# Performance work log

Measured on AMD Instinct MI355X. Metric: run time of the kernel, lower is better.

Reference implementation:

```python
import jax, jax.numpy as jnp
import numpy as np

BATCH = 32768
TEXT_DIM = 384
HIDDEN = 256
NUM_LAYERS = 4
NUM_VERTS = 12
K_NN = 6


def _build_template():
    """Icosphere vertices (12, normalized) and row-normalized kNN adjacency (12,12)."""
    phi = (1.0 + 5.0 ** 0.5) / 2.0
    v = np.array([
        [-1, phi, 0], [1, phi, 0], [-1, -phi, 0], [1, -phi, 0],
        [0, -1, phi], [0, 1, phi], [0, -1, -phi], [0, 1, -phi],
        [phi, 0, -1], [phi, 0, 1], [-phi, 0, -1], [-phi, 0, 1],
    ], dtype=np.float32)
    v = v / np.linalg.norm(v, axis=1, keepdims=True)
    dist = np.linalg.norm(v[:, None, :] - v[None, :, :], axis=-1)  # (12,12)
    # k+1 smallest per row; index 0 is self (distance 0), skip it
    idx = np.argsort(dist, axis=1, kind='stable')[:, 1:K_NN + 1]
    adj = np.zeros((NUM_VERTS, NUM_VERTS), dtype=np.float32)
    rows = np.repeat(np.arange(NUM_VERTS), K_NN)
    adj[rows, idx.reshape(-1)] = 1.0
    adj = adj / (adj.sum(axis=1, keepdims=True) + 1e-6)
    return jnp.asarray(v), jnp.asarray(adj)


def setup_inputs() -> dict:
    key = jax.random.key(0)
    ks = jax.random.split(key, 8)
    template, adjacency = _build_template()
    scale = 0.02
    return {
        "text_emb": jax.random.normal(ks[0], (BATCH, TEXT_DIM), dtype=jnp.float32),
        "W_text": jax.random.normal(ks[1], (TEXT_DIM, HIDDEN), dtype=jnp.float32) * scale,
        "b_text": jnp.zeros((HIDDEN,), dtype=jnp.float32),
        "W_gnn": jax.random.normal(ks[2], (NUM_LAYERS, HIDDEN, HIDDEN), dtype=jnp.float32) * scale,
        "b_gnn": jnp.zeros((NUM_LAYERS, HIDDEN), dtype=jnp.float32),
        "W_out": jax.random.normal(ks[3], (HIDDEN, 3), dtype=jnp.float32) * scale,
        "b_out": jnp.zeros((3,), dtype=jnp.float32),
        "adjacency": adjacency,   # (12,12) buffer
        "template": template,     # (12,3) buffer
    }


def reference(text_emb, W_text, b_text, W_gnn, b_gnn, W_out, b_out, adjacency, template):
    # text projection -> broadcast to all nodes
    tf = text_emb @ W_text + b_text                       # (B, H)
    B = text_emb.shape[0]
    h = jnp.broadcast_to(tf[:, None, :], (B, NUM_VERTS, HIDDEN))
    # GNN layers: aggregate (shared adjacency across batch), project, relu
    for l in range(NUM_LAYERS):
        agg = jnp.einsum('nm,bmd->bnd', adjacency, h)     # (B, 12, H)
        h = jax.nn.relu(agg @ W_gnn[l] + b_gnn[l])
    displacements = h @ W_out + b_out                     # (B, 12, 3)
    return template[None, :, :] + displacements
```

## Files before the change

### kernel.cpp

```cpp
#include <hip/hip_runtime.h>
#include <stdint.h>

#define TD      384
#define HID     256
#define NLAYERS 4

typedef __bf16 bf16;
typedef __attribute__((ext_vector_type(8))) __bf16 bf16x8;
typedef __attribute__((ext_vector_type(4))) float f32x4;

union FragU { uint4 u; bf16x8 f; };
union PackU { uint4 u; bf16 v[8]; };

__device__ inline f32x4 mfma16(bf16x8 a, bf16x8 b, f32x4 c) {
  return __builtin_amdgcn_mfma_f32_16x16x32_bf16(a, b, c, 0, 0, 0);
}

__global__ __launch_bounds__(256) void prep_kernel(
    const float* __restrict__ W_text, const float* __restrict__ W_gnn,
    const float* __restrict__ W_out,
    bf16* __restrict__ wt_text, bf16* __restrict__ wt_gnn, float* __restrict__ wot)
{
  int bid = blockIdx.x, tid = threadIdx.x;
  if (bid < 48) {
    int idx = bid * 256 + tid;
    int cc = idx & 15, c = idx >> 4;
    int n16 = c / 48, oct = c - n16 * 48;
    int n = n16 * 16 + cc;
    PackU pk;
    #pragma unroll
    for (int j = 0; j < 8; j++) pk.v[j] = (bf16)W_text[(oct * 8 + j) * HID + n];
    *(uint4*)(wt_text + idx * 8) = pk.u;
  } else if (bid < 176) {
    int idx = (bid - 48) * 256 + tid;
    int cc = idx & 15, c = idx >> 4;
    int l = c >> 9, c2 = c & 511;
    int oct = c2 & 31;
    int n = (c2 >> 5) * 16 + cc;
    const float* base = W_gnn + l * HID * HID;
    PackU pk;
    #pragma unroll
    for (int j = 0; j < 8; j++) pk.v[j] = (bf16)base[(oct * 8 + j) * HID + n];
    *(uint4*)(wt_gnn + idx * 8) = pk.u;
  } else {
    for (int t = tid; t < 3 * HID; t += 256) {
      int comp = t >> 8, k = t & 255;
      wot[comp * HID + k] = W_out[k * 3 + comp];
    }
  }
}

__global__ __launch_bounds__(256, 2) void mesh_kernel(
    const float* __restrict__ text,
    const bf16* __restrict__ wt_text,
    const bf16* __restrict__ wt_gnn,
    const float* __restrict__ b_text,
    const float* __restrict__ b_gnn,
    const float* __restrict__ wot,
    const float* __restrict__ b_out,
    const float* __restrict__ tmpl,
    float* __restrict__ out)
{
  __shared__ __align__(16) unsigned char smem[81920];
  unsigned char* Tbuf = smem;
  unsigned char* Hbuf = smem + 49152;

  const int tid  = threadIdx.x;
  const int lane = tid & 63;
  const int w    = tid >> 6;
  const int cc   = lane & 15;
  const int qq   = lane >> 4;
  const int rowbase = blockIdx.x * 64;

  f32x4 acc[4][4];

  {
    const float* tbase = text + (size_t)rowbase * TD;
    #pragma unroll
    for (int i = 0; i < 12; i++) {
      int id = i * 256 + tid;
      int m = id / 48, o = id - m * 48;
      const float4* p = (const float4*)(tbase + m * TD + o * 8);
      float4 x = p[0], y = p[1];
      PackU pk;
      pk.v[0]=(bf16)x.x; pk.v[1]=(bf16)x.y; pk.v[2]=(bf16)x.z; pk.v[3]=(bf16)x.w;
      pk.v[4]=(bf16)y.x; pk.v[5]=(bf16)y.y; pk.v[6]=(bf16)y.z; pk.v[7]=(bf16)y.w;
      *(uint4*)(Tbuf + m * 768 + (o ^ (m & 7)) * 16) = pk.u;
    }
  }
  __syncthreads();

  auto zero_acc = [&]() {
    f32x4 z = {0.f, 0.f, 0.f, 0.f};
    #pragma unroll
    for (int mt = 0; mt < 4; mt++)
      #pragma unroll
      for (int nt = 0; nt < 4; nt++) acc[mt][nt] = z;
  };

  auto loadA = [&](const unsigned char* src, int rowB, int ks, bf16x8* A) {
    #pragma unroll
    for (int mt = 0; mt < 4; mt++) {
      int m = mt * 16 + cc;
      FragU fu;
      fu.u = *(const uint4*)(src + m * rowB + (((ks * 4 + qq) ^ (m & 7)) * 16));
      A[mt] = fu.f;
    }
  };

  auto loadB = [&](const char* wb, int K8, int ks, bf16x8* B) {
    #pragma unroll
    for (int nt = 0; nt < 4; nt++) {
      FragU fu;
      fu.u = *(const uint4*)(wb + (size_t)(nt * K8 + ks * 4) * 256);
      B[nt] = fu.f;
    }
  };

  auto runLayer = [&](const unsigned char* src, int rowB, int nks,
                      const char* wb, int K8,
                      unsigned char* dst, const float* bias_ptr, bool relu) {
    zero_acc();
    bf16x8 A[4], B[4], An[4], Bn[4];
    loadB(wb, K8, 0, B);
    loadA(src, rowB, 0, A);
    #pragma unroll
    for (int ks = 0; ks < nks; ks++) {
      if (ks + 1 < nks) {
        loadB(wb, K8, ks + 1, Bn);
        loadA(src, rowB, ks + 1, An);
      }
      #pragma unroll
      for (int mt = 0; mt < 4; mt++)
        #pragma unroll
        for (int nt = 0; nt < 4; nt++)
          acc[mt][nt] = mfma16(A[mt], B[nt], acc[mt][nt]);
      if (ks + 1 < nks) {
        #pragma unroll
        for (int t = 0; t < 4; t++) { A[t] = An[t]; B[t] = Bn[t]; }
      }
    }
    float bias4[4];
    #pragma unroll
    for (int nt = 0; nt < 4; nt++) bias4[nt] = bias_ptr[w * 64 + nt * 16 + cc];
    #pragma unroll
    for (int mt = 0; mt < 4; mt++) {
      #pragma unroll
      for (int nt = 0; nt < 4; nt++) {
        int col = w * 64 + nt * 16 + cc;
        #pragma unroll
        for (int r = 0; r < 4; r++) {
          int m = mt * 16 + qq * 4 + r;
          float v = acc[mt][nt][r] + bias4[nt];
          if (relu) v = fmaxf(v, 0.f);
          *(bf16*)(dst + m * 512 + ((col >> 3) ^ (m & 7)) * 16 + (col & 7) * 2) = (bf16)v;
        }
      }
    }
  };

  const char* wb0 = (const char*)wt_text + (size_t)(w * 4 * 48 + qq) * 256 + cc * 16;

  runLayer(Tbuf, 768, TD / 32, wb0, 48, Hbuf, b_text, false);
  __syncthreads();

  #pragma unroll
  for (int l = 0; l < NLAYERS; l++) {
    const unsigned char* src = (l & 1) ? Tbuf : Hbuf;
    unsigned char*       dst = (l & 1) ? Hbuf : Tbuf;
    const char* wb = (const char*)(wt_gnn) + (size_t)l * HID * HID * 2
                   + (size_t)(w * 4 * 32 + qq) * 256 + cc * 16;
    runLayer(src, 512, HID / 32, wb, 32, dst, b_gnn + l * HID, true);
    __syncthreads();
  }

  float* dispBuf = (float*)Tbuf;

  if (tid < 192) {
    int comp = tid >> 6;
    int r = tid & 63;
    const float4* wrow = (const float4*)(wot + comp * HID);
    float s = 0.f;
    #pragma unroll 4
    for (int o = 0; o < 32; o++) {
      FragU fu; fu.u = *(const uint4*)(Hbuf + r * 512 + ((o ^ (r & 7)) * 16));
      float4 w0 = wrow[2 * o], w1 = wrow[2 * o + 1];
      s += (float)fu.f[0]*w0.x + (float)fu.f[1]*w0.y + (float)fu.f[2]*w0.z + (float)fu.f[3]*w0.w;
      s += (float)fu.f[4]*w1.x + (float)fu.f[5]*w1.y + (float)fu.f[6]*w1.z + (float)fu.f[7]*w1.w;
    }
    dispBuf[r * 3 + comp] = s + b_out[comp];
  }
  __syncthreads();

  #pragma unroll
  for (int ii = 0; ii < 9; ii++) {
    int i = ii * 256 + tid;
    int row = i / 36;
    int j = i - row * 36;
    out[(size_t)rowbase * 36 + i] = tmpl[j] + dispBuf[row * 3 + j % 3];
  }
}

extern "C" void kernel_launch(void* const* d_in, const int* in_sizes, int n_in,
                              void* d_out, int out_size, void* d_ws, size_t ws_size,
                              hipStream_t stream) {
  const float* text   = (const float*)d_in[0];
  const float* W_text = (const float*)d_in[1];
  const float* b_text = (const float*)d_in[2];
  const float* W_gnn  = (const float*)d_in[3];
  const float* b_gnn  = (const float*)d_in[4];
  const float* W_out  = (const float*)d_in[5];
  const float* b_out  = (const float*)d_in[6];
  const float* tmpl   = (const float*)d_in[8];
  float* outp = (float*)d_out;

  bf16* wt_text = (bf16*)d_ws;
  bf16* wt_gnn  = wt_text + 256*384;
  float* wot    = (float*)(wt_gnn + 4*256*256);

  prep_kernel<<<177, 256, 0, stream>>>(W_text, W_gnn, W_out, wt_text, wt_gnn, wot);
  mesh_kernel<<<32768/64, 256, 0, stream>>>(text, wt_text, wt_gnn, b_text, b_gnn,
                                            wot, b_out, tmpl, outp);
}
```

Measured before the change: 125.1 us.

## Fold text projection into first GNN layer and pipeline text staging

After: 151.1 us. 1.21x slower.

```diff
diff --git a/kernel.cpp b/kernel.cpp
--- a/kernel.cpp
+++ b/kernel.cpp
@@ -3,7 +3,6 @@
 
 #define TD      384
 #define HID     256
-#define NLAYERS 4
 
 typedef __bf16 bf16;
 typedef __attribute__((ext_vector_type(8))) __bf16 bf16x8;
@@ -16,10 +15,40 @@
   return __builtin_amdgcn_mfma_f32_16x16x32_bf16(a, b, c, 0, 0, 0);
 }
 
-__global__ __launch_bounds__(256) void prep_kernel(
-    const float* __restrict__ W_text, const float* __restrict__ W_gnn,
+__global__ __launch_bounds__(256) void prep_wf(
+    const float* __restrict__ W_text, const float* __restrict__ b_text,
+    const float* __restrict__ W_gnn, const float* __restrict__ b_gnn,
+    float* __restrict__ wf, float* __restrict__ bfv)
+{
+  int n = threadIdx.x;
+  int k = blockIdx.x;
+  const float* g0 = W_gnn;
+  if (k < TD) {
+    const float* trow = W_text + (size_t)k * HID;
+    float a0 = 0.f, a1 = 0.f, a2 = 0.f, a3 = 0.f;
+    for (int j = 0; j < HID; j += 4) {
+      a0 += trow[j]     * g0[(j    ) * HID + n];
+      a1 += trow[j + 1] * g0[(j + 1) * HID + n];
+      a2 += trow[j + 2] * g0[(j + 2) * HID + n];
+      a3 += trow[j + 3] * g0[(j + 3) * HID + n];
+    }
+    wf[(size_t)k * HID + n] = (a0 + a1) + (a2 + a3);
+  } else {
+    float a0 = 0.f, a1 = 0.f, a2 = 0.f, a3 = 0.f;
+    for (int j = 0; j < HID; j += 4) {
+      a0 += b_text[j]     * g0[(j    ) * HID + n];
+      a1 += b_text[j + 1] * g0[(j + 1) * HID + n];
+      a2 += b_text[j + 2] * g0[(j + 2) * HID + n];
+      a3 += b_text[j + 3] * g0[(j + 3) * HID + n];
+    }
+    bfv[n] = (a0 + a1) + (a2 + a3) + b_gnn[n];
+  }
+}
+
+__global__ __launch_bounds__(256) void prep_pack(
+    const float* __restrict__ wf, const float* __restrict__ W_gnn,
     const float* __restrict__ W_out,
-    bf16* __restrict__ wt_text, bf16* __restrict__ wt_gnn, float* __restrict__ wot)
+    bf16* __restrict__ wt_f, bf16* __restrict__ wt_g, float* __restrict__ wot)
 {
   int bid = blockIdx.x, tid = threadIdx.x;
   if (bid < 48) {
@@ -29,19 +58,19 @@
     int n = n16 * 16 + cc;
     PackU pk;
     #pragma unroll
-    for (int j = 0; j < 8; j++) pk.v[j] = (bf16)W_text[(oct * 8 + j) * HID + n];
-    *(uint4*)(wt_text + idx * 8) = pk.u;
-  } else if (bid < 176) {
+    for (int j = 0; j < 8; j++) pk.v[j] = (bf16)wf[(oct * 8 + j) * HID + n];
+    *(uint4*)(wt_f + idx * 8) = pk.u;
+  } else if (bid < 144) {
     int idx = (bid - 48) * 256 + tid;
     int cc = idx & 15, c = idx >> 4;
     int l = c >> 9, c2 = c & 511;
     int oct = c2 & 31;
     int n = (c2 >> 5) * 16 + cc;
-    const float* base = W_gnn + l * HID * HID;
+    const float* base = W_gnn + (size_t)(l + 1) * HID * HID;
     PackU pk;
     #pragma unroll
     for (int j = 0; j < 8; j++) pk.v[j] = (bf16)base[(oct * 8 + j) * HID + n];
-    *(uint4*)(wt_gnn + idx * 8) = pk.u;
+    *(uint4*)(wt_g + idx * 8) = pk.u;
   } else {
     for (int t = tid; t < 3 * HID; t += 256) {
       int comp = t >> 8, k = t & 255;
@@ -50,20 +79,20 @@
   }
 }
 
-__global__ __launch_bounds__(256, 2) void mesh_kernel(
+__global__ __launch_bounds__(256, 3) void mesh_kernel(
     const float* __restrict__ text,
-    const bf16* __restrict__ wt_text,
-    const bf16* __restrict__ wt_gnn,
-    const float* __restrict__ b_text,
+    const bf16* __restrict__ wt_f,
+    const bf16* __restrict__ wt_g,
+    const float* __restrict__ b_f,
     const float* __restrict__ b_gnn,
     const float* __restrict__ wot,
     const float* __restrict__ b_out,
     const float* __restrict__ tmpl,
     float* __restrict__ out)
 {
-  __shared__ __align__(16) unsigned char smem[81920];
+  __shared__ __align__(16) unsigned char smem[49920];
   unsigned char* Tbuf = smem;
-  unsigned char* Hbuf = smem + 49152;
+  float* dispBuf = (float*)(smem + 49152);
 
   const int tid  = threadIdx.x;
   const int lane = tid & 63;
@@ -74,22 +103,6 @@
 
   f32x4 acc[4][4];
 
-  {
-    const float* tbase = text + (size_t)rowbase * TD;
-    #pragma unroll
-    for (int i = 0; i < 12; i++) {
-      int id = i * 256 + tid;
-      int m = id / 48, o = id - m * 48;
-      const float4* p = (const float4*)(tbase + m * TD + o * 8);
-      float4 x = p[0], y = p[1];
-      PackU pk;
-      pk.v[0]=(bf16)x.x; pk.v[1]=(bf16)x.y; pk.v[2]=(bf16)x.z; pk.v[3]=(bf16)x.w;
-      pk.v[4]=(bf16)y.x; pk.v[5]=(bf16)y.y; pk.v[6]=(bf16)y.z; pk.v[7]=(bf16)y.w;
-      *(uint4*)(Tbuf + m * 768 + (o ^ (m & 7)) * 16) = pk.u;
-    }
-  }
-  __syncthreads();
-
   auto zero_acc = [&]() {
     f32x4 z = {0.f, 0.f, 0.f, 0.f};
     #pragma unroll
@@ -117,29 +130,7 @@
     }
   };
 
-  auto runLayer = [&](const unsigned char* src, int rowB, int nks,
-                      const char* wb, int K8,
-                      unsigned char* dst, const float* bias_ptr, bool relu) {
-    zero_acc();
-    bf16x8 A[4], B[4], An[4], Bn[4];
-    loadB(wb, K8, 0, B);
-    loadA(src, rowB, 0, A);
-    #pragma unroll
-    for (int ks = 0; ks < nks; ks++) {
-      if (ks + 1 < nks) {
-        loadB(wb, K8, ks + 1, Bn);
-        loadA(src, rowB, ks + 1, An);
-      }
-      #pragma unroll
-      for (int mt = 0; mt < 4; mt++)
-        #pragma unroll
-        for (int nt = 0; nt < 4; nt++)
-          acc[mt][nt] = mfma16(A[mt], B[nt], acc[mt][nt]);
-      if (ks + 1 < nks) {
-        #pragma unroll
-        for (int t = 0; t < 4; t++) { A[t] = An[t]; B[t] = Bn[t]; }
-      }
-    }
+  auto epilogue = [&](const float* bias_ptr, bool relu) {
     float bias4[4];
     #pragma unroll
     for (int nt = 0; nt < 4; nt++) bias4[nt] = bias_ptr[w * 64 + nt * 16 + cc];
@@ -153,28 +144,100 @@
           int m = mt * 16 + qq * 4 + r;
           float v = acc[mt][nt][r] + bias4[nt];
           if (relu) v = fmaxf(v, 0.f);
-          *(bf16*)(dst + m * 512 + ((col >> 3) ^ (m & 7)) * 16 + (col & 7) * 2) = (bf16)v;
+          *(bf16*)(Tbuf + m * 512 + ((col >> 3) ^ (m & 7)) * 16 + (col & 7) * 2) = (bf16)v;
         }
       }
     }
   };
 
-  const char* wb0 = (const char*)wt_text + (size_t)(w * 4 * 48 + qq) * 256 + cc * 16;
-
-  runLayer(Tbuf, 768, TD / 32, wb0, 48, Hbuf, b_text, false);
+  const float* tbase = text + (size_t)rowbase * TD;
+  float4 pf[6];
+
+  auto stageLoad = [&](int c) {
+    #pragma unroll
+    for (int i = 0; i < 3; i++) {
+      int id = i * 256 + tid;
+      int m = id / 12, ol = id - m * 12;
+      const float4* p = (const float4*)(tbase + m * TD + (c * 12 + ol) * 8);
+      pf[2 * i]     = p[0];
+      pf[2 * i + 1] = p[1];
+    }
+  };
+  auto stageWrite = [&](int c) {
+    #pragma unroll
+    for (int i = 0; i < 3; i++) {
+      int id = i * 256 + tid;
+      int m = id / 12, ol = id - m * 12;
+      int o = c * 12 + ol;
+      float4 x = pf[2 * i], y = pf[2 * i + 1];
+      PackU pk;
+      pk.v[0]=(bf16)x.x; pk.v[1]=(bf16)x.y; pk.v[2]=(bf16)x.z; pk.v[3]=(bf16)x.w;
+      pk.v[4]=(bf16)y.x; pk.v[5]=(bf16)y.y; pk.v[6]=(bf16)y.z; pk.v[7]=(bf16)y.w;
+      *(uint4*)(Tbuf + m * 768 + ((o ^ (m & 7)) * 16)) = pk.u;
+    }
+  };
+
+  zero_acc();
+  stageLoad(0);
+  stageWrite(0);
   __syncthreads();
 
-  #pragma unroll
-  for (int l = 0; l < NLAYERS; l++) {
-    const unsigned char* src = (l & 1) ? Tbuf : Hbuf;
-    unsigned char*       dst = (l & 1) ? Hbuf : Tbuf;
-    const char* wb = (const char*)(wt_gnn) + (size_t)l * HID * HID * 2
+  const char* wbf = (const char*)wt_f + (size_t)(w * 4 * 48 + qq) * 256 + cc * 16;
+  {
+    bf16x8 B[4], Bn[4];
+    loadB(wbf, 48, 0, B);
+    for (int c = 0; c < 4; c++) {
+      if (c < 3) stageLoad(c + 1);
+      #pragma unroll
+      for (int k2 = 0; k2 < 3; k2++) {
+        int ks = c * 3 + k2;
+        if (ks < 11) loadB(wbf, 48, ks + 1, Bn);
+        bf16x8 A[4];
+        loadA(Tbuf, 768, ks, A);
+        #pragma unroll
+        for (int mt = 0; mt < 4; mt++)
+          #pragma unroll
+          for (int nt = 0; nt < 4; nt++)
+            acc[mt][nt] = mfma16(A[mt], B[nt], acc[mt][nt]);
+        if (ks < 11) {
+          #pragma unroll
+          for (int t = 0; t < 4; t++) B[t] = Bn[t];
+        }
+      }
+      if (c < 3) stageWrite(c + 1);
+      __syncthreads();
+    }
+  }
+  epilogue(b_f, true);
+  __syncthreads();
+
+  for (int l = 0; l < 3; l++) {
+    const char* wb = (const char*)wt_g + (size_t)l * HID * HID * 2
                    + (size_t)(w * 4 * 32 + qq) * 256 + cc * 16;
-    runLayer(src, 512, HID / 32, wb, 32, dst, b_gnn + l * HID, true);
+    zero_acc();
+    bf16x8 A[4], B[4], An[4], Bn[4];
+    loadB(wb, 32, 0, B);
+    loadA(Tbuf, 512, 0, A);
+    #pragma unroll
+    for (int ks = 0; ks < 8; ks++) {
+      if (ks < 7) {
+        loadB(wb, 32, ks + 1, Bn);
+        loadA(Tbuf, 512, ks + 1, An);
+      }
+      #pragma unroll
+      for (int mt = 0; mt < 4; mt++)
+        #pragma unroll
+        for (int nt = 0; nt < 4; nt++)
+          acc[mt][nt] = mfma16(A[mt], B[nt], acc[mt][nt]);
+      if (ks < 7) {
+        #pragma unroll
+        for (int t = 0; t < 4; t++) { A[t] = An[t]; B[t] = Bn[t]; }
+      }
+    }
     __syncthreads();
-  }
-
-  float* dispBuf = (float*)Tbuf;
+    epilogue(b_gnn + (l + 1) * HID, true);
+    __syncthreads();
+  }
 
   if (tid < 192) {
     int comp = tid >> 6;
@@ -183,7 +246,7 @@
     float s = 0.f;
     #pragma unroll 4
     for (int o = 0; o < 32; o++) {
-      FragU fu; fu.u = *(const uint4*)(Hbuf + r * 512 + ((o ^ (r & 7)) * 16));
+      FragU fu; fu.u = *(const uint4*)(Tbuf + r * 512 + ((o ^ (r & 7)) * 16));
       float4 w0 = wrow[2 * o], w1 = wrow[2 * o + 1];
       s += (float)fu.f[0]*w0.x + (float)fu.f[1]*w0.y + (float)fu.f[2]*w0.z + (float)fu.f[3]*w0.w;
       s += (float)fu.f[4]*w1.x + (float)fu.f[5]*w1.y + (float)fu.f[6]*w1.z + (float)fu.f[7]*w1.w;
@@ -214,11 +277,14 @@
   const float* tmpl   = (const float*)d_in[8];
   float* outp = (float*)d_out;
 
-  bf16* wt_text = (bf16*)d_ws;
-  bf16* wt_gnn  = wt_text + 256*384;
-  float* wot    = (float*)(wt_gnn + 4*256*256);
-
-  prep_kernel<<<177, 256, 0, stream>>>(W_text, W_gnn, W_out, wt_text, wt_gnn, wot);
-  mesh_kernel<<<32768/64, 256, 0, stream>>>(text, wt_text, wt_gnn, b_text, b_gnn,
-                                            wot, b_out, tmpl, outp);
-}
+  float* wf   = (float*)d_ws;
+  float* bfv  = wf + TD * HID;
+  float* wot  = bfv + HID;
+  bf16* wt_f  = (bf16*)(wot + 3 * HID);
+  bf16* wt_g  = wt_f + TD * HID;
+
+  prep_wf<<<TD + 1, 256, 0, stream>>>(W_text, b_text, W_gnn, b_gnn, wf, bfv);
+  prep_pack<<<145, 256, 0, stream>>>(wf, W_gnn, W_out, wt_f, wt_g, wot);
+  mesh_kernel<<<32768 / 64, 256, 0, stream>>>(text, wt_f, wt_g, bfv, b_gnn,
+                                              wot, b_out, tmpl, outp);
+}
```
